# Kernel tuning notes

Hardware: AMD Instinct MI355X
Metric: run time of the kernel (lower is better)

## Reference

```python
import jax, jax.numpy as jnp
import numpy as np

NUM_HEADS = 8

def _qkv(t, W, b, H):
    # t: [B, L, C] -> q, k, v each [B, H, L, D]
    B, L, C = t.shape
    D = C // H
    qkv = (t @ W + b).reshape(B, L, 3, H, D)
    qkv = jnp.moveaxis(qkv, 2, 0)           # [3, B, L, H, D]
    qkv = jnp.swapaxes(qkv, 2, 3)           # [3, B, H, L, D]
    return qkv[0], qkv[1], qkv[2]

def _attend(q, k, v, scale):
    # q,k,v: [B, H, L, D] -> [B, L, C]
    B, H, L, D = q.shape
    scores = jnp.einsum('bhqd,bhkd->bhqk', q, k) * scale
    attn = jax.nn.softmax(scores, axis=-1)
    out = jnp.einsum('bhqk,bhkd->bhqd', attn, v)
    return jnp.swapaxes(out, 1, 2).reshape(B, L, H * D)

def setup_inputs() -> dict:
    key = jax.random.key(0)
    ks = jax.random.split(key, 7)
    B, N, C = 8, 2048, 512
    s_in = 1.0 / np.sqrt(C)
    return {
        'x': jax.random.normal(ks[0], (B, N, C), dtype=jnp.float32),
        'W_rgb_qkv': jax.random.normal(ks[1], (C, 3 * C), dtype=jnp.float32) * s_in,
        'b_rgb_qkv': jax.random.normal(ks[2], (3 * C,), dtype=jnp.float32) * 0.02,
        'W_depth_qkv': jax.random.normal(ks[3], (C, 3 * C), dtype=jnp.float32) * s_in,
        'b_depth_qkv': jax.random.normal(ks[4], (3 * C,), dtype=jnp.float32) * 0.02,
        'W_proj': jax.random.normal(ks[5], (C, C), dtype=jnp.float32) * s_in,
        'b_proj': jax.random.normal(ks[6], (C,), dtype=jnp.float32) * 0.02,
    }

def reference(x, W_rgb_qkv, b_rgb_qkv, W_depth_qkv, b_depth_qkv, W_proj, b_proj):
    B, N, C = x.shape
    H = NUM_HEADS
    D = C // H
    scale = D ** -0.5
    L = N // 2
    rgb, depth = x[:, :L], x[:, L:]
    rq, rk, rv = _qkv(rgb, W_rgb_qkv, b_rgb_qkv, H)
    dq, dk, dv = _qkv(depth, W_depth_qkv, b_depth_qkv, H)
    # rgb queries attend to depth K/V (named depth_v in torch code)
    depth_out = _attend(rq, dk, dv, scale)
    # depth queries attend to rgb K/V (named rgb_v in torch code)
    rgb_out = _attend(dq, rk, rv, scale)
    out = jnp.concatenate([rgb_out, depth_out], axis=1)  # [B, N, C]
    return out @ W_proj + b_proj
```

## Files before the change

### kernel.cpp

```cpp
#include <hip/hip_runtime.h>
#include <hip/hip_bf16.h>

typedef __attribute__((ext_vector_type(8))) short s16x8;
typedef __attribute__((ext_vector_type(4))) float f32x4;

__device__ __forceinline__ ushort f2bf(float f) {
  union { float f; unsigned int u; } c; c.f = f;
  unsigned int u = c.u + 0x7fffu + ((c.u >> 16) & 1u);
  return (ushort)(u >> 16);
}

__device__ __forceinline__ unsigned int pack2(float lo, float hi) {
  __hip_bfloat162 b2 = __float22bfloat162_rn(make_float2(lo, hi));
  union { __hip_bfloat162 b; unsigned int u; } c; c.b = b2;
  return c.u;
}

__device__ __forceinline__ s16x8 ld16(const ushort* p) {
  union { uint4 u; s16x8 s; } c;
  c.u = *reinterpret_cast<const uint4*>(p);
  return c.s;
}

__device__ __forceinline__ f32x4 mfma16(s16x8 a, s16x8 b, f32x4 c) {
  return __builtin_amdgcn_mfma_f32_16x16x32_bf16(a, b, c, 0, 0, 0);
}

__device__ __forceinline__ float exp2fast(float x) { return __builtin_amdgcn_exp2f(x); }

__device__ __forceinline__ void gld_lds16(const void* g, void* l) {
  __builtin_amdgcn_global_load_lds(
      (const __attribute__((address_space(1))) void*)g,
      (__attribute__((address_space(3))) void*)l, 16, 0, 0);
}


__global__ __launch_bounds__(256) void k_prep(
    const float* __restrict__ x, ushort* __restrict__ xb,
    const float* __restrict__ Wr, ushort* __restrict__ WtR,
    const float* __restrict__ Wd, ushort* __restrict__ WtD,
    const float* __restrict__ Wp, ushort* __restrict__ WtP) {
  __shared__ float tile[32][33];
  int b = blockIdx.x, t = threadIdx.x;
  if (b < 8192) {
    int i = (b * 256 + t) * 4;
    float4 v = *reinterpret_cast<const float4*>(x + i);
    ushort4 o;
    o.x = f2bf(v.x); o.y = f2bf(v.y); o.z = f2bf(v.z); o.w = f2bf(v.w);
    *reinterpret_cast<ushort4*>(xb + i) = o;
    return;
  }
  b -= 8192;
  const float* src; ushort* dst; int N;
  if (b < 768)      { src = Wr; dst = WtR; N = 1536; }
  else if (b < 1536){ b -= 768;  src = Wd; dst = WtD; N = 1536; }
  else              { b -= 1536; src = Wp; dst = WtP; N = 512; }
  int nb = N >> 5;
  int n0 = (b % nb) * 32, k0 = (b / nb) * 32;
  int tx = t & 31, ty = t >> 5;
#pragma unroll
  for (int i = 0; i < 32; i += 8)
    tile[ty + i][tx] = src[(k0 + ty + i) * N + (n0 + tx)];
  __syncthreads();
#pragma unroll
  for (int i = 0; i < 32; i += 8)
    dst[(size_t)(n0 + ty + i) * 512 + (k0 + tx)] = f2bf(tile[tx][ty + i]);
}


__device__ __forceinline__ void stage_lds(const ushort* __restrict__ src, int ld,
                                          char* ldsbase, int t) {
#pragma unroll
  for (int p = 0; p < 4; ++p) {
    int chunk = p * 256 + t;
    int r = chunk >> 3, cc = chunk & 7;
    gld_lds16(src + r * ld + ((cc ^ (r & 7)) * 8), ldsbase + (chunk & ~63) * 16);
  }
}

__device__ __forceinline__ s16x8 lds_frag(const char* lds, int row, int c) {
  union { uint4 u; s16x8 s; } cv;
  cv.u = *reinterpret_cast<const uint4*>(lds + row * 128 + ((c ^ (row & 7)) * 16));
  return cv.s;
}


template <bool TRANS>
__global__ __launch_bounds__(256) void k_qkv(
    const ushort* __restrict__ xb, const ushort* __restrict__ WtR,
    const ushort* __restrict__ WtD, const float* __restrict__ bR,
    const float* __restrict__ bD, ushort* __restrict__ Qb,
    ushort* __restrict__ Kb, ushort* __restrict__ Vt) {
  __shared__ __align__(16) char lds[65536];
  int m0 = blockIdx.x * 128;
  int n0 = (TRANS ? 1024 : 0) + blockIdx.y * 128;
  int s = m0 >> 13, bb = (m0 >> 10) & 7, lbase = m0 & 1023;
  const ushort* A = xb + (size_t)(bb * 2048 + s * 1024 + lbase) * 512;
  const ushort* Wt = (s ? WtD : WtR) + (size_t)n0 * 512;
  const float* bias = s ? bD : bR;
  int t = threadIdx.x;
  int wid = t >> 6, ln = t & 15, g = (t & 63) >> 4;
  int wr = wid >> 1, wc = wid & 1;
  f32x4 acc[4][4] = {};
  stage_lds(A, 512, lds, t);
  stage_lds(Wt, 512, lds + 16384, t);
  __syncthreads();
  for (int ks = 0; ks < 8; ++ks) {
    char* cbuf = lds + (ks & 1) * 32768;
    if (ks < 7) {
      char* nbuf = lds + ((ks + 1) & 1) * 32768;
      stage_lds(A + (ks + 1) * 64, 512, nbuf, t);
      stage_lds(Wt + (ks + 1) * 64, 512, nbuf + 16384, t);
    }
    char* ldsA = cbuf;
    char* ldsB = cbuf + 16384;
#pragma unroll
    for (int kk = 0; kk < 2; ++kk) {
      s16x8 af[4], bf[4];
#pragma unroll
      for (int mi = 0; mi < 4; ++mi) af[mi] = lds_frag(ldsA, wr * 64 + mi * 16 + ln, kk * 4 + g);
#pragma unroll
      for (int ni = 0; ni < 4; ++ni) bf[ni] = lds_frag(ldsB, wc * 64 + ni * 16 + ln, kk * 4 + g);
#pragma unroll
      for (int mi = 0; mi < 4; ++mi)
#pragma unroll
        for (int ni = 0; ni < 4; ++ni)
          acc[mi][ni] = TRANS ? mfma16(bf[ni], af[mi], acc[mi][ni])
                              : mfma16(af[mi], bf[ni], acc[mi][ni]);
    }
    __syncthreads();
  }
  int hb_base = (s * 8 + bb) * 8;
  if (!TRANS) {
    bool isK = (n0 >> 9) != 0;
    ushort* dst = isK ? Kb : Qb;
    float sc = isK ? 1.0f : 0.18033688011112042f;
#pragma unroll
    for (int mi = 0; mi < 4; ++mi)
#pragma unroll
      for (int ni = 0; ni < 4; ++ni) {
        f32x4 v = acc[mi][ni];
        int col = n0 + wc * 64 + ni * 16 + ln;
        int h = (col >> 6) & 7, d = col & 63;
        float bv = bias[col];
        ushort* hp = dst + ((size_t)(hb_base + h) << 16);
        int lr = lbase + wr * 64 + mi * 16 + g * 4;
#pragma unroll
        for (int j = 0; j < 4; ++j) hp[(lr + j) * 64 + d] = f2bf((v[j] + bv) * sc);
      }
  } else {
#pragma unroll
    for (int mi = 0; mi < 4; ++mi)
#pragma unroll
      for (int ni = 0; ni < 4; ++ni) {
        f32x4 v = acc[mi][ni];
        int nb = n0 + wc * 64 + ni * 16 + g * 4;
        int mm = m0 + wr * 64 + mi * 16 + ln;
        int l = mm & 1023;
        int lp = (l & ~63) | (l & 0x23) | ((l & 0x0C) << 1) | ((l & 0x10) >> 2);
#pragma unroll
        for (int j = 0; j < 4; ++j) {
          int col = nb + j;
          int h = (col >> 6) & 7, d = col & 63;
          Vt[((size_t)(hb_base + h) << 16) + d * 1024 + lp] = f2bf(v[j] + bias[col]);
        }
      }
  }
}


__global__ __launch_bounds__(256) void k_attn(const ushort* __restrict__ Qb,
                                              const ushort* __restrict__ Kb,
                                              const ushort* __restrict__ Vt,
                                              ushort* __restrict__ AO) {
  __shared__ __align__(16) char lds[40960];
  int bid = blockIdx.x;
  int set = bid & 127, qb = bid >> 7;
  int pair = set & 1, h = (set >> 1) & 7, bb = set >> 4;
  int sQ = 1 - pair, sKV = pair;
  const ushort* Qp = Qb + ((size_t)((sQ * 8 + bb) * 8 + h) << 16);
  const ushort* Kp = Kb + ((size_t)((sKV * 8 + bb) * 8 + h) << 16);
  const ushort* Vp = Vt + ((size_t)((sKV * 8 + bb) * 8 + h) << 16);
  int t = threadIdx.x, w = t >> 6, l = t & 63, ln = t & 15, g = (t & 63) >> 4;
  int q0 = qb * 128 + w * 32;
  s16x8 qf0a = ld16(Qp + (q0 + ln) * 64 + g * 8);
  s16x8 qf1a = ld16(Qp + (q0 + ln) * 64 + 32 + g * 8);
  s16x8 qf0b = ld16(Qp + (q0 + 16 + ln) * 64 + g * 8);
  s16x8 qf1b = ld16(Qp + (q0 + 16 + ln) * 64 + 32 + g * 8);

  int cA = w * 128 + l;
  int cB = w * 128 + 64 + l;
  int rA = cA >> 3, ccA = cA & 7;
  int rB = cB >> 3, ccB = cB & 7;
  int kofA = rA * 64 + ((ccA ^ (rA & 7)) * 8);
  int kofB = rB * 64 + ((ccB ^ (rB & 7)) * 8);
  int vofA = rA * 1024 + ((ccA ^ (rA & 7)) * 8);
  int vofB = rB * 1024 + ((ccB ^ (rB & 7)) * 8);

  float ls_a = 0.f, ls_b = 0.f;
  f32x4 oca[4] = {}, ocb[4] = {};

  const ushort* kstage = Kp;
  const ushort* vstage = Vp;

  char* kc = lds;
  char* kn = lds + 8192;
  char* ks = lds + 16384;
  char* vc = lds + 24576;
  char* vn = lds + 32768;

  gld_lds16(kstage + kofA, kc + w * 2048);
  gld_lds16(kstage + kofB, kc + w * 2048 + 1024);
  kstage += 4096;
  gld_lds16(kstage + kofA, kn + w * 2048);
  gld_lds16(kstage + kofB, kn + w * 2048 + 1024);
  kstage += 4096;
  gld_lds16(vstage + vofA, vc + w * 2048);
  gld_lds16(vstage + vofB, vc + w * 2048 + 1024);
  vstage += 64;
  asm volatile("s_waitcnt vmcnt(4)" ::: "memory");
  __builtin_amdgcn_sched_barrier(0);
  __builtin_amdgcn_s_barrier();
  __builtin_amdgcn_sched_barrier(0);

  for (int it = 0; it < 16; ++it) {
    if (it < 14) {
      gld_lds16(kstage + kofA, ks + w * 2048);
      gld_lds16(kstage + kofB, ks + w * 2048 + 1024);
      kstage += 4096;
    }
    if (it < 15) {
      gld_lds16(vstage + vofA, vn + w * 2048);
      gld_lds16(vstage + vofB, vn + w * 2048 + 1024);
      vstage += 64;
    }

    f32x4 za[4], zb[4];
    __builtin_amdgcn_s_setprio(1);
#pragma unroll
    for (int s = 0; s < 4; ++s) {
      s16x8 k0 = lds_frag(kc, s * 16 + ln, g);
      s16x8 k1 = lds_frag(kc, s * 16 + ln, 4 + g);
      f32x4 z1 = {}; z1 = mfma16(k0, qf0a, z1); z1 = mfma16(k1, qf1a, z1); za[s] = z1;
      f32x4 z2 = {}; z2 = mfma16(k0, qf0b, z2); z2 = mfma16(k1, qf1b, z2); zb[s] = z2;
    }
    __builtin_amdgcn_s_setprio(0);

    unsigned int pwa[8], pwb[8];
#pragma unroll
    for (int s = 0; s < 4; ++s) {
      float p0 = exp2fast(za[s][0]), p1 = exp2fast(za[s][1]);
      float p2 = exp2fast(za[s][2]), p3 = exp2fast(za[s][3]);
      ls_a += (p0 + p1) + (p2 + p3);
      pwa[2 * s] = pack2(p0, p1); pwa[2 * s + 1] = pack2(p2, p3);
      float r0 = exp2fast(zb[s][0]), r1 = exp2fast(zb[s][1]);
      float r2 = exp2fast(zb[s][2]), r3 = exp2fast(zb[s][3]);
      ls_b += (r0 + r1) + (r2 + r3);
      pwb[2 * s] = pack2(r0, r1); pwb[2 * s + 1] = pack2(r2, r3);
    }
    union { uint4 u; s16x8 v; } c0, c1, c2, c3;
    c0.u = make_uint4(pwa[0], pwa[1], pwa[2], pwa[3]);
    c1.u = make_uint4(pwa[4], pwa[5], pwa[6], pwa[7]);
    c2.u = make_uint4(pwb[0], pwb[1], pwb[2], pwb[3]);
    c3.u = make_uint4(pwb[4], pwb[5], pwb[6], pwb[7]);
    s16x8 pf0a = c0.v, pf1a = c1.v, pf0b = c2.v, pf1b = c3.v;

    if (it < 14) {
      asm volatile("s_waitcnt vmcnt(4)" ::: "memory");
    } else if (it == 14) {
      asm volatile("s_waitcnt vmcnt(2)" ::: "memory");
    } else {
      asm volatile("s_waitcnt vmcnt(0)" ::: "memory");
    }
    __builtin_amdgcn_sched_barrier(0);

    __builtin_amdgcn_s_setprio(1);
#pragma unroll
    for (int d = 0; d < 4; ++d) {
      s16x8 v0 = lds_frag(vc, d * 16 + ln, g);
      s16x8 v1 = lds_frag(vc, d * 16 + ln, 4 + g);
      oca[d] = mfma16(v0, pf0a, oca[d]);
      oca[d] = mfma16(v1, pf1a, oca[d]);
      ocb[d] = mfma16(v0, pf0b, ocb[d]);
      ocb[d] = mfma16(v1, pf1b, ocb[d]);
    }
    __builtin_amdgcn_s_setprio(0);

    if (it < 15) {
      __builtin_amdgcn_sched_barrier(0);
      __builtin_amdgcn_s_barrier();
      __builtin_amdgcn_sched_barrier(0);
    }
    char* tmp = kc; kc = kn; kn = ks; ks = tmp;
    char* tv = vc; vc = vn; vn = tv;
  }

  ls_a += __shfl_xor(ls_a, 16, 64);
  ls_a += __shfl_xor(ls_a, 32, 64);
  ls_b += __shfl_xor(ls_b, 16, 64);
  ls_b += __shfl_xor(ls_b, 32, 64);
  float inva = 1.0f / ls_a, invb = 1.0f / ls_b;
  int orow = bb * 2048 + pair * 1024 + q0 + ln;
#pragma unroll
  for (int d = 0; d < 4; ++d) {
    uint2 st;
    st.x = pack2(oca[d][0] * inva, oca[d][1] * inva);
    st.y = pack2(oca[d][2] * inva, oca[d][3] * inva);
    *reinterpret_cast<uint2*>(AO + (size_t)orow * 512 + h * 64 + d * 16 + 4 * g) = st;
    uint2 st2;
    st2.x = pack2(ocb[d][0] * invb, ocb[d][1] * invb);
    st2.y = pack2(ocb[d][2] * invb, ocb[d][3] * invb);
    *reinterpret_cast<uint2*>(AO + (size_t)(orow + 16) * 512 + h * 64 + d * 16 + 4 * g) = st2;
  }
}


__global__ __launch_bounds__(256) void k_gemm_proj(const ushort* __restrict__ AO,
                                                   const ushort* __restrict__ WtP,
                                                   const float* __restrict__ bP,
                                                   float* __restrict__ Out) {
  __shared__ __align__(16) char lds[65536];
  int m0 = blockIdx.x * 128, n0 = blockIdx.y * 128;
  const ushort* A = AO + (size_t)m0 * 512;
  const ushort* Wt = WtP + (size_t)n0 * 512;
  int t = threadIdx.x;
  int wid = t >> 6, ln = t & 15, g = (t & 63) >> 4;
  int wr = wid >> 1, wc = wid & 1;
  f32x4 acc[4][4] = {};
  stage_lds(A, 512, lds, t);
  stage_lds(Wt, 512, lds + 16384, t);
  __syncthreads();
  for (int ks = 0; ks < 8; ++ks) {
    char* cbuf = lds + (ks & 1) * 32768;
    if (ks < 7) {
      char* nbuf = lds + ((ks + 1) & 1) * 32768;
      stage_lds(A + (ks + 1) * 64, 512, nbuf, t);
      stage_lds(Wt + (ks + 1) * 64, 512, nbuf + 16384, t);
    }
    char* ldsA = cbuf;
    char* ldsB = cbuf + 16384;
#pragma unroll
    for (int kk = 0; kk < 2; ++kk) {
      s16x8 af[4], bf[4];
#pragma unroll
      for (int mi = 0; mi < 4; ++mi) af[mi] = lds_frag(ldsA, wr * 64 + mi * 16 + ln, kk * 4 + g);
#pragma unroll
      for (int ni = 0; ni < 4; ++ni) bf[ni] = lds_frag(ldsB, wc * 64 + ni * 16 + ln, kk * 4 + g);
#pragma unroll
      for (int mi = 0; mi < 4; ++mi)
#pragma unroll
        for (int ni = 0; ni < 4; ++ni) acc[mi][ni] = mfma16(af[mi], bf[ni], acc[mi][ni]);
    }
    __syncthreads();
  }
#pragma unroll
  for (int mi = 0; mi < 4; ++mi)
#pragma unroll
    for (int ni = 0; ni < 4; ++ni) {
      f32x4 v = acc[mi][ni];
      int col = n0 + wc * 64 + ni * 16 + ln;
      float bv = bP[col];
      int r0 = m0 + wr * 64 + mi * 16 + g * 4;
#pragma unroll
      for (int j = 0; j < 4; ++j) Out[(size_t)(r0 + j) * 512 + col] = v[j] + bv;
    }
}


extern "C" void kernel_launch(void* const* d_in, const int* in_sizes, int n_in,
                              void* d_out, int out_size, void* d_ws, size_t ws_size,
                              hipStream_t stream) {
  const float* x      = (const float*)d_in[0];
  const float* W_rgb  = (const float*)d_in[1];
  const float* b_rgb  = (const float*)d_in[2];
  const float* W_dep  = (const float*)d_in[3];
  const float* b_dep  = (const float*)d_in[4];
  const float* W_proj = (const float*)d_in[5];
  const float* b_proj = (const float*)d_in[6];
  float* out = (float*)d_out;

  char* ws = (char*)d_ws;
  ushort* xb  = (ushort*)(ws + 0);
  ushort* WtR = (ushort*)(ws + 16777216);
  ushort* WtD = (ushort*)(ws + 18350080);
  ushort* WtP = (ushort*)(ws + 19922944);
  ushort* Qb  = (ushort*)(ws + 20447232);
  ushort* Kb  = (ushort*)(ws + 37224448);
  ushort* Vt  = (ushort*)(ws + 54001664);
  ushort* AO  = (ushort*)(ws + 70778880);

  k_prep<<<9984, 256, 0, stream>>>(x, xb, W_rgb, WtR, W_dep, WtD, W_proj, WtP);
  k_qkv<false><<<dim3(128, 8), 256, 0, stream>>>(xb, WtR, WtD, b_rgb, b_dep, Qb, Kb, Vt);
  k_qkv<true><<<dim3(128, 4), 256, 0, stream>>>(xb, WtR, WtD, b_rgb, b_dep, Qb, Kb, Vt);
  k_attn<<<1024, 256, 0, stream>>>(Qb, Kb, Vt, AO);
  k_gemm_proj<<<dim3(128, 4), 256, 0, stream>>>(AO, WtP, b_proj, out);
}
```

Baseline: 144.5 us.

## Use 512-thread attention blocks with 256 queries and double-buffered K/V

The attention kernel now launches 512 blocks of 8 waves, each covering 256 queries instead of 128. Each K/V tile loaded into LDS is therefore reused by twice as many queries, and each thread loads one 16-byte chunk per tile. The three-deep K pipeline with fine-grained vmcnt waits becomes a plain double buffer that waits for all loads (vmcnt(0)) before the barrier. This cuts LDS use and global K/V traffic, but it exposes more load latency per iteration and uses a 512-thread barrier. It also relies on the block index decode (set = bid&127, qb = bid>>7) still covering all query tiles with 512 blocks.

```diff
diff --git a/kernel.cpp b/kernel.cpp
--- a/kernel.cpp
+++ b/kernel.cpp
@@ -169,11 +169,11 @@
 }
 
 
-__global__ __launch_bounds__(256) void k_attn(const ushort* __restrict__ Qb,
+__global__ __launch_bounds__(512) void k_attn(const ushort* __restrict__ Qb,
                                               const ushort* __restrict__ Kb,
                                               const ushort* __restrict__ Vt,
                                               ushort* __restrict__ AO) {
-  __shared__ __align__(16) char lds[40960];
+  __shared__ __align__(16) char lds[32768];
   int bid = blockIdx.x;
   int set = bid & 127, qb = bid >> 7;
   int pair = set & 1, h = (set >> 1) & 7, bb = set >> 4;
@@ -181,21 +181,17 @@
   const ushort* Qp = Qb + ((size_t)((sQ * 8 + bb) * 8 + h) << 16);
   const ushort* Kp = Kb + ((size_t)((sKV * 8 + bb) * 8 + h) << 16);
   const ushort* Vp = Vt + ((size_t)((sKV * 8 + bb) * 8 + h) << 16);
-  int t = threadIdx.x, w = t >> 6, l = t & 63, ln = t & 15, g = (t & 63) >> 4;
-  int q0 = qb * 128 + w * 32;
+  int t = threadIdx.x, w = t >> 6, ln = t & 15, g = (t & 63) >> 4;
+  int q0 = qb * 256 + w * 32;
   s16x8 qf0a = ld16(Qp + (q0 + ln) * 64 + g * 8);
   s16x8 qf1a = ld16(Qp + (q0 + ln) * 64 + 32 + g * 8);
   s16x8 qf0b = ld16(Qp + (q0 + 16 + ln) * 64 + g * 8);
   s16x8 qf1b = ld16(Qp + (q0 + 16 + ln) * 64 + 32 + g * 8);
 
-  int cA = w * 128 + l;
-  int cB = w * 128 + 64 + l;
-  int rA = cA >> 3, ccA = cA & 7;
-  int rB = cB >> 3, ccB = cB & 7;
-  int kofA = rA * 64 + ((ccA ^ (rA & 7)) * 8);
-  int kofB = rB * 64 + ((ccB ^ (rB & 7)) * 8);
-  int vofA = rA * 1024 + ((ccA ^ (rA & 7)) * 8);
-  int vofB = rB * 1024 + ((ccB ^ (rB & 7)) * 8);
+  int r = t >> 3, cc = t & 7;
+  int kof = r * 64 + ((cc ^ (r & 7)) * 8);
+  int vof = r * 1024 + ((cc ^ (r & 7)) * 8);
+  int ldst = (t & ~63) * 16;
 
   float ls_a = 0.f, ls_b = 0.f;
   f32x4 oca[4] = {}, ocb[4] = {};
@@ -204,35 +200,23 @@
   const ushort* vstage = Vp;
 
   char* kc = lds;
-  char* kn = lds + 8192;
-  char* ks = lds + 16384;
-  char* vc = lds + 24576;
-  char* vn = lds + 32768;
-
-  gld_lds16(kstage + kofA, kc + w * 2048);
-  gld_lds16(kstage + kofB, kc + w * 2048 + 1024);
-  kstage += 4096;
-  gld_lds16(kstage + kofA, kn + w * 2048);
-  gld_lds16(kstage + kofB, kn + w * 2048 + 1024);
-  kstage += 4096;
-  gld_lds16(vstage + vofA, vc + w * 2048);
-  gld_lds16(vstage + vofB, vc + w * 2048 + 1024);
-  vstage += 64;
-  asm volatile("s_waitcnt vmcnt(4)" ::: "memory");
+  char* vc = lds + 8192;
+  char* kn = lds + 16384;
+  char* vn = lds + 24576;
+
+  gld_lds16(kstage + kof, kc + ldst);
+  gld_lds16(vstage + vof, vc + ldst);
+  kstage += 4096; vstage += 64;
+  asm volatile("s_waitcnt vmcnt(0)" ::: "memory");
   __builtin_amdgcn_sched_barrier(0);
   __builtin_amdgcn_s_barrier();
   __builtin_amdgcn_sched_barrier(0);
 
   for (int it = 0; it < 16; ++it) {
-    if (it < 14) {
-      gld_lds16(kstage + kofA, ks + w * 2048);
-      gld_lds16(kstage + kofB, ks + w * 2048 + 1024);
-      kstage += 4096;
-    }
     if (it < 15) {
-      gld_lds16(vstage + vofA, vn + w * 2048);
-      gld_lds16(vstage + vofB, vn + w * 2048 + 1024);
-      vstage += 64;
+      gld_lds16(kstage + kof, kn + ldst);
+      gld_lds16(vstage + vof, vn + ldst);
+      kstage += 4096; vstage += 64;
     }
 
     f32x4 za[4], zb[4];
@@ -265,15 +249,6 @@
     c3.u = make_uint4(pwb[4], pwb[5], pwb[6], pwb[7]);
     s16x8 pf0a = c0.v, pf1a = c1.v, pf0b = c2.v, pf1b = c3.v;
 
-    if (it < 14) {
-      asm volatile("s_waitcnt vmcnt(4)" ::: "memory");
-    } else if (it == 14) {
-      asm volatile("s_waitcnt vmcnt(2)" ::: "memory");
-    } else {
-      asm volatile("s_waitcnt vmcnt(0)" ::: "memory");
-    }
-    __builtin_amdgcn_sched_barrier(0);
-
     __builtin_amdgcn_s_setprio(1);
 #pragma unroll
     for (int d = 0; d < 4; ++d) {
@@ -287,11 +262,12 @@
     __builtin_amdgcn_s_setprio(0);
 
     if (it < 15) {
+      asm volatile("s_waitcnt vmcnt(0)" ::: "memory");
       __builtin_amdgcn_sched_barrier(0);
       __builtin_amdgcn_s_barrier();
       __builtin_amdgcn_sched_barrier(0);
     }
-    char* tmp = kc; kc = kn; kn = ks; ks = tmp;
+    char* tk = kc; kc = kn; kn = tk;
     char* tv = vc; vc = vn; vn = tv;
   }
 
@@ -392,6 +368,6 @@
   k_prep<<<9984, 256, 0, stream>>>(x, xb, W_rgb, WtR, W_dep, WtD, W_proj, WtP);
   k_qkv<false><<<dim3(128, 8), 256, 0, stream>>>(xb, WtR, WtD, b_rgb, b_dep, Qb, Kb, Vt);
   k_qkv<true><<<dim3(128, 4), 256, 0, stream>>>(xb, WtR, WtD, b_rgb, b_dep, Qb, Kb, Vt);
-  k_attn<<<1024, 256, 0, stream>>>(Qb, Kb, Vt, AO);
+  k_attn<<<512, 512, 0, stream>>>(Qb, Kb, Vt, AO);
   k_gemm_proj<<<dim3(128, 4), 256, 0, stream>>>(AO, WtP, b_proj, out);
 }
```

New measurement: 137.1 us. -5.1%, faster.
